# Performance work log

Measured on AMD Instinct MI355X. Metric: run time of the kernel, lower is better.

The kernel has to match this reference:

```python
import jax, jax.numpy as jnp
import numpy as np

HIDDEN = 32  # hidden_size


def setup_inputs() -> dict:
    key = jax.random.key(0)
    kx, kwx, kwh = jax.random.split(key, 3)
    B, T, F = 256, 2048, 64
    x = jax.random.normal(kx, (B, T, F), dtype=jnp.float32)
    # Flax OptimizedLSTMCell params: input kernel (no bias) and hidden kernel (with bias),
    # gate order (i, f, g, o), each of width HIDDEN -> concatenated 4*HIDDEN.
    Wx = jax.random.normal(kwx, (F, 4 * HIDDEN), dtype=jnp.float32) / np.sqrt(F)
    Wh = jax.random.normal(kwh, (HIDDEN, 4 * HIDDEN), dtype=jnp.float32) / np.sqrt(HIDDEN)
    b = jnp.zeros((4 * HIDDEN,), dtype=jnp.float32)
    return {"x": x, "Wx": Wx, "Wh": Wh, "b": b}


def _lstm(x, Wx, Wh, b):
    B, T, F = x.shape
    H = Wh.shape[0]
    # Precompute input contribution for all timesteps (same math, one big GEMM).
    xg = jnp.einsum("btf,fg->btg", x, Wx) + b  # [B, T, 4H]
    xg = xg.swapaxes(0, 1)  # [T, B, 4H] for scan over time
    c0 = jnp.zeros((B, H), dtype=x.dtype)
    h0 = jnp.zeros((B, H), dtype=x.dtype)

    def step(carry, xg_t):
        c, h = carry
        gates = xg_t + h @ Wh  # [B, 4H]
        i, f, g, o = jnp.split(gates, 4, axis=-1)  # flax gate order: i, f, g, o
        c_new = jax.nn.sigmoid(f) * c + jax.nn.sigmoid(i) * jnp.tanh(g)
        h_new = jax.nn.sigmoid(o) * jnp.tanh(c_new)
        return (c_new, h_new), h_new

    _, ys = jax.lax.scan(step, (c0, h0), xg)  # ys: [T, B, H]
    return ys.swapaxes(0, 1)  # [B, T, H]


def reference(x, Wx, Wh, b):
    return _lstm(x, Wx, Wh, b)
```

## Files before the change

kernel.cpp:

```cpp
#include <hip/hip_runtime.h>
#include <hip/hip_fp16.h>

#define BB 256
#define TT 2048
#define FF 64
#define HH 32
#define G4 128
#define K2E 1.4426950408889634f

typedef float f32x2 __attribute__((ext_vector_type(2)));

__device__ __forceinline__ float fast_rcp(float x){ return __builtin_amdgcn_rcpf(x); }
__device__ __forceinline__ float fast_exp2(float x){
#if __has_builtin(__builtin_amdgcn_exp2f)
  return __builtin_amdgcn_exp2f(x);
#else
  return exp2f(x);
#endif
}
__device__ __forceinline__ void swap_halves(float &a, float &b){
#if __has_builtin(__builtin_amdgcn_permlane32_swap)
  typedef int i32x2_ __attribute__((ext_vector_type(2)));
  i32x2_ r = __builtin_amdgcn_permlane32_swap(__float_as_int(a), __float_as_int(b), false, false);
  a = __int_as_float(r.x);
  b = __int_as_float(r.y);
#else
  asm("v_permlane32_swap_b32 %0, %1" : "+v"(a), "+v"(b));
#endif
}

#define PKFMA_VV(acc, a, b) asm("v_pk_fma_f32 %0, %1, %2, %0" : "+v"(acc) : "v"(a), "v"(b))
#define DOT2_SV(acc, hs, wv) asm("v_dot2_f32_f16 %0, %1, %2, %0" : "+v"(acc) : "s"(hs), "v"(wv))

__global__ __launch_bounds__(256) void lstm_gemm(const float* __restrict__ x,
    const float* __restrict__ Wx, const float* __restrict__ bias,
    float* __restrict__ xg, int t0, int ct)
{
  __shared__ float sW[FF*G4];
  __shared__ float sB[G4];
  __shared__ float sX[64*68];
  int tid = threadIdx.x;
  {
    const float4* Wx4 = (const float4*)Wx;
    float4* sW4 = (float4*)sW;
#pragma unroll
    for (int q=0;q<8;q++) sW4[q*256+tid] = Wx4[q*256+tid];
    if (tid < 32) ((float4*)sB)[tid] = ((const float4*)bias)[tid];
  }
  long total = (long)BB*ct;
  long m0 = (long)blockIdx.x * 64;
#pragma unroll
  for (int s=0;s<4;s++){
    int idx = tid + s*256;
    int row = idx >> 4, q = idx & 15;
    long gm = m0 + row;
    float4 v = make_float4(0.f,0.f,0.f,0.f);
    if (gm < total){
      int bidx = (int)((unsigned long)gm / (unsigned)ct);
      int tt   = (int)(gm - (long)bidx*ct);
      v = ((const float4*)(x + ((size_t)bidx*TT + t0 + tt)*FF))[q];
    }
    *(float4*)&sX[row*68 + q*4] = v;
  }
  __syncthreads();
  int rg = tid >> 5;
  int cg = tid & 31;
  int r0 = rg*8;
  f32x2 acc[8][4];
#pragma unroll
  for (int r=0;r<8;r++)
#pragma unroll
    for (int c=0;c<4;c++) acc[r][c] = (f32x2){0.f,0.f};
#pragma unroll 8
  for (int kp=0; kp<32; kp++){
    int k = kp*2;
    f32x2 xv[8];
#pragma unroll
    for (int r=0;r<8;r++) xv[r] = *(const f32x2*)&sX[(r0+r)*68 + k];
    f32x2 wv[4];
#pragma unroll
    for (int c=0;c<4;c++){
      f32x2 w; w.x = sW[k*G4 + cg + 32*c]; w.y = sW[(k+1)*G4 + cg + 32*c];
      wv[c] = w;
    }
#pragma unroll
    for (int r=0;r<8;r++)
#pragma unroll
      for (int c=0;c<4;c++) PKFMA_VV(acc[r][c], xv[r], wv[c]);
  }
#pragma unroll
  for (int r=0;r<8;r++){
    long gm = m0 + r0 + r;
    if (gm < total){
      f32x2* o = (f32x2*)(xg + (size_t)gm*G4);
      f32x2 p0, p1;
      p0.x = (acc[r][0].x + acc[r][0].y + sB[cg])      * (-K2E);
      p0.y = (acc[r][1].x + acc[r][1].y + sB[cg+32])   * (-K2E);
      p1.x = (acc[r][2].x + acc[r][2].y + sB[cg+64])   * (2.f*K2E);
      p1.y = (acc[r][3].x + acc[r][3].y + sB[cg+96])   * (-K2E);
      o[cg]      = p0;
      o[cg + 32] = p1;
    }
  }
}

__global__ __launch_bounds__(64)
__attribute__((amdgpu_waves_per_eu(1,1)))
void lstm_scan(const float* __restrict__ xg,
    const float* __restrict__ Wh, float* __restrict__ ys,
    float* __restrict__ state, int t0, int ct)
{
  int r = blockIdx.x;
  int l = threadIdx.x;
  int j = l & 31;
  int half = l >> 5;
  int base = j + half*64;

  float ws0 = half ? (2.f*K2E) : (-K2E);
  float ws1 = -K2E;
  unsigned wh0[16], wh1[16];
#pragma unroll
  for (int kk=0;kk<16;kk++){
    __half2 a  = __floats2half2_rn(Wh[(2*kk)*G4 + base]*ws0,    Wh[(2*kk+1)*G4 + base]*ws0);
    __half2 b_ = __floats2half2_rn(Wh[(2*kk)*G4 + base+32]*ws1, Wh[(2*kk+1)*G4 + base+32]*ws1);
    wh0[kk] = *(unsigned*)&a;
    wh1[kk] = *(unsigned*)&b_;
  }
#pragma unroll
  for (int kk=0;kk<16;kk++){ asm volatile("" : "+v"(wh0[kk]), "+v"(wh1[kk])); }

  float A0 = half ? -2.f : 1.f;
  float B0 = half ?  1.f : 0.f;

  float da = (float)half, db = (float)half;
  swap_halves(da, db);
  bool flip = (da != 0.0f);

  float cc, hcur;
  if (t0 == 0){ cc = 0.f; hcur = 0.f; }
  else { cc = state[r*HH + j]; hcur = state[BB*HH + r*HH + j]; }

  const f32x2* xq = (const f32x2*)(xg + (size_t)r*ct*G4) + l;
  float* yp = ys + ((size_t)r*TT + t0)*HH;

  auto STEP = [&](f32x2 xv, int t){
    float hn = __int_as_float(__builtin_amdgcn_update_dpp(
        0, __float_as_int(hcur), 0xB1 , 0xF, 0xF, true));
    __half2 pk2 = __floats2half2_rn(hcur, hn);
    int pk = *(int*)&pk2;
    int hp[16];
#pragma unroll
    for (int kk=0;kk<16;kk++) hp[kk] = __builtin_amdgcn_readlane(pk, 2*kk);
    float cA = xv.x, cB = 0.f, dA = xv.y, dB = 0.f;
#pragma unroll
    for (int kk=0;kk<8;kk++){
      DOT2_SV(cA, hp[kk],   wh0[kk]);
      DOT2_SV(dA, hp[kk],   wh1[kk]);
      DOT2_SV(cB, hp[kk+8], wh0[kk+8]);
      DOT2_SV(dB, hp[kk+8], wh1[kk+8]);
    }
    float g0 = cA + cB;
    float g1 = dA + dB;
    float t1v = fast_rcp(1.f + fast_exp2(g1));
    float t0v = fmaf(A0, fast_rcp(1.f + fast_exp2(g0)), B0);
    float si = t0v, tg = t0v;
    swap_halves(si, tg);
    float ig = si * tg;
    float e0 = t1v, e1 = t1v;
    swap_halves(e0, e1);
    float sf = flip ? e1 : e0;
    float so = flip ? e0 : e1;
    cc = fmaf(sf, cc, ig);
    float tc = fmaf(-2.f, fast_rcp(1.f + fast_exp2((2.f*K2E)*cc)), 1.f);
    hcur = so * tc;
    if (half == 0) yp[(size_t)t*HH + j] = hcur;
  };

  f32x2 bufA[8], bufB[8];
#pragma unroll
  for (int u=0;u<8;u++){ int t_ = (u < ct) ? u : (ct-1); bufA[u] = xq[(size_t)t_*64]; }

  int tb = 0;
  for (; tb + 16 <= ct; tb += 16){
#pragma unroll
    for (int u=0;u<8;u++) bufB[u] = xq[(size_t)(tb+8+u)*64];
#pragma unroll
    for (int u=0;u<8;u++) STEP(bufA[u], tb+u);
#pragma unroll
    for (int u=0;u<8;u++){ int t_ = tb+16+u; if (t_ > ct-1) t_ = ct-1; bufA[u] = xq[(size_t)t_*64]; }
#pragma unroll
    for (int u=0;u<8;u++) STEP(bufB[u], tb+8+u);
  }
  for (int t=tb; t<ct; ++t) STEP(xq[(size_t)t*64], t);

  if (half == 0){
    state[r*HH + j] = cc;
    state[BB*HH + r*HH + j] = hcur;
  }
}

extern "C" void kernel_launch(void* const* d_in, const int* in_sizes, int n_in,
                              void* d_out, int out_size, void* d_ws, size_t ws_size,
                              hipStream_t stream)
{
  const float* x  = (const float*)d_in[0];
  const float* Wx = (const float*)d_in[1];
  const float* Wh = (const float*)d_in[2];
  const float* b  = (const float*)d_in[3];
  float* ys = (float*)d_out;
  char* ws = (char*)d_ws;
  float* state = (float*)ws;
  float* xg = (float*)(ws + 65536);
  size_t per_step = (size_t)BB * G4 * sizeof(float);
  size_t avail = ws_size > 65536 ? ws_size - 65536 : 0;
  long ctl = (long)(avail / per_step);
  int CT = (ctl >= TT) ? TT : (int)ctl;
  if (CT < 1) CT = 1;
  for (int t0 = 0; t0 < TT; t0 += CT){
    int ct = (TT - t0 < CT) ? (TT - t0) : CT;
    int wgs = (int)(((long)BB*ct + 63)/64);
    lstm_gemm<<<dim3(wgs), dim3(256), 0, stream>>>(x, Wx, b, xg, t0, ct);
    lstm_scan<<<dim3(BB), dim3(64), 0, stream>>>(xg, Wh, ys, state, t0, ct);
  }
}
```

Baseline: 526.0 us.

## Process two batch rows per scan wavefront to interleave independent recurrences

```diff
diff --git a/kernel.cpp b/kernel.cpp
--- a/kernel.cpp
+++ b/kernel.cpp
@@ -110,7 +110,8 @@
     const float* __restrict__ Wh, float* __restrict__ ys,
     float* __restrict__ state, int t0, int ct)
 {
-  int r = blockIdx.x;
+  int rA = blockIdx.x * 2;
+  int rB = rA + 1;
   int l = threadIdx.x;
   int j = l & 31;
   int half = l >> 5;
@@ -136,67 +137,99 @@
   swap_halves(da, db);
   bool flip = (da != 0.0f);
 
-  float cc, hcur;
-  if (t0 == 0){ cc = 0.f; hcur = 0.f; }
-  else { cc = state[r*HH + j]; hcur = state[BB*HH + r*HH + j]; }
-
-  const f32x2* xq = (const f32x2*)(xg + (size_t)r*ct*G4) + l;
-  float* yp = ys + ((size_t)r*TT + t0)*HH;
-
-  auto STEP = [&](f32x2 xv, int t){
+  float ccA, hA, ccB, hB;
+  if (t0 == 0){ ccA = hA = ccB = hB = 0.f; }
+  else {
+    ccA = state[rA*HH + j];  hA = state[BB*HH + rA*HH + j];
+    ccB = state[rB*HH + j];  hB = state[BB*HH + rB*HH + j];
+  }
+
+  const f32x2* xqA = (const f32x2*)(xg + (size_t)rA*ct*G4) + l;
+  const f32x2* xqB = (const f32x2*)(xg + (size_t)rB*ct*G4) + l;
+  float* ypS = ys + ((size_t)(rA+half)*TT + t0)*HH + j;
+
+  auto PACK = [&](float h)->int{
     float hn = __int_as_float(__builtin_amdgcn_update_dpp(
-        0, __float_as_int(hcur), 0xB1 , 0xF, 0xF, true));
-    __half2 pk2 = __floats2half2_rn(hcur, hn);
-    int pk = *(int*)&pk2;
-    int hp[16];
-#pragma unroll
-    for (int kk=0;kk<16;kk++) hp[kk] = __builtin_amdgcn_readlane(pk, 2*kk);
-    float cA = xv.x, cB = 0.f, dA = xv.y, dB = 0.f;
+        0, __float_as_int(h), 0xB1 , 0xF, 0xF, true));
+    __half2 pk2 = __floats2half2_rn(h, hn);
+    return *(int*)&pk2;
+  };
+
+  auto STEP2 = [&](f32x2 xa, f32x2 xb, int t){
+    int pkA = PACK(hA);
+    int pkB = PACK(hB);
+    int hpA[16], hpB[16];
+#pragma unroll
+    for (int kk=0;kk<16;kk++){
+      hpA[kk] = __builtin_amdgcn_readlane(pkA, 2*kk);
+      hpB[kk] = __builtin_amdgcn_readlane(pkB, 2*kk);
+    }
+    float cA0=xa.x, cA1=0.f, dA0=xa.y, dA1=0.f;
+    float cB0=xb.x, cB1=0.f, dB0=xb.y, dB1=0.f;
 #pragma unroll
     for (int kk=0;kk<8;kk++){
-      DOT2_SV(cA, hp[kk],   wh0[kk]);
-      DOT2_SV(dA, hp[kk],   wh1[kk]);
-      DOT2_SV(cB, hp[kk+8], wh0[kk+8]);
-      DOT2_SV(dB, hp[kk+8], wh1[kk+8]);
-    }
-    float g0 = cA + cB;
-    float g1 = dA + dB;
-    float t1v = fast_rcp(1.f + fast_exp2(g1));
-    float t0v = fmaf(A0, fast_rcp(1.f + fast_exp2(g0)), B0);
-    float si = t0v, tg = t0v;
-    swap_halves(si, tg);
-    float ig = si * tg;
-    float e0 = t1v, e1 = t1v;
-    swap_halves(e0, e1);
-    float sf = flip ? e1 : e0;
-    float so = flip ? e0 : e1;
-    cc = fmaf(sf, cc, ig);
-    float tc = fmaf(-2.f, fast_rcp(1.f + fast_exp2((2.f*K2E)*cc)), 1.f);
-    hcur = so * tc;
-    if (half == 0) yp[(size_t)t*HH + j] = hcur;
+      DOT2_SV(cA0, hpA[kk],   wh0[kk]);
+      DOT2_SV(dA0, hpA[kk],   wh1[kk]);
+      DOT2_SV(cB0, hpB[kk],   wh0[kk]);
+      DOT2_SV(dB0, hpB[kk],   wh1[kk]);
+      DOT2_SV(cA1, hpA[kk+8], wh0[kk+8]);
+      DOT2_SV(dA1, hpA[kk+8], wh1[kk+8]);
+      DOT2_SV(cB1, hpB[kk+8], wh0[kk+8]);
+      DOT2_SV(dB1, hpB[kk+8], wh1[kk+8]);
+    }
+    float g0A = cA0+cA1, g1A = dA0+dA1;
+    float g0B = cB0+cB1, g1B = dB0+dB1;
+    float t1A = fast_rcp(1.f + fast_exp2(g1A));
+    float t1B = fast_rcp(1.f + fast_exp2(g1B));
+    float t0A = fmaf(A0, fast_rcp(1.f + fast_exp2(g0A)), B0);
+    float t0B = fmaf(A0, fast_rcp(1.f + fast_exp2(g0B)), B0);
+    float siA = t0A, tgA = t0A; swap_halves(siA, tgA);
+    float siB = t0B, tgB = t0B; swap_halves(siB, tgB);
+    float igA = siA * tgA;
+    float igB = siB * tgB;
+    float e0A = t1A, e1A = t1A; swap_halves(e0A, e1A);
+    float e0B = t1B, e1B = t1B; swap_halves(e0B, e1B);
+    float sfA = flip ? e1A : e0A, soA = flip ? e0A : e1A;
+    float sfB = flip ? e1B : e0B, soB = flip ? e0B : e1B;
+    ccA = fmaf(sfA, ccA, igA);
+    ccB = fmaf(sfB, ccB, igB);
+    float tcA = fmaf(-2.f, fast_rcp(1.f + fast_exp2((2.f*K2E)*ccA)), 1.f);
+    float tcB = fmaf(-2.f, fast_rcp(1.f + fast_exp2((2.f*K2E)*ccB)), 1.f);
+    hA = soA * tcA;
+    hB = soB * tcB;
+    ypS[(size_t)t*HH] = half ? hB : hA;
   };
 
-  f32x2 bufA[8], bufB[8];
-#pragma unroll
-  for (int u=0;u<8;u++){ int t_ = (u < ct) ? u : (ct-1); bufA[u] = xq[(size_t)t_*64]; }
-
+  f32x2 aA[4], aB[4], bA[4], bB[4];
+#pragma unroll
+  for (int u=0;u<4;u++){
+    int t_ = (u < ct) ? u : (ct-1);
+    aA[u] = xqA[(size_t)t_*64];
+    aB[u] = xqB[(size_t)t_*64];
+  }
   int tb = 0;
-  for (; tb + 16 <= ct; tb += 16){
-#pragma unroll
-    for (int u=0;u<8;u++) bufB[u] = xq[(size_t)(tb+8+u)*64];
-#pragma unroll
-    for (int u=0;u<8;u++) STEP(bufA[u], tb+u);
-#pragma unroll
-    for (int u=0;u<8;u++){ int t_ = tb+16+u; if (t_ > ct-1) t_ = ct-1; bufA[u] = xq[(size_t)t_*64]; }
-#pragma unroll
-    for (int u=0;u<8;u++) STEP(bufB[u], tb+8+u);
-  }
-  for (int t=tb; t<ct; ++t) STEP(xq[(size_t)t*64], t);
-
-  if (half == 0){
-    state[r*HH + j] = cc;
-    state[BB*HH + r*HH + j] = hcur;
-  }
+  for (; tb + 8 <= ct; tb += 8){
+#pragma unroll
+    for (int u=0;u<4;u++){
+      int t_ = tb + 4 + u;
+      bA[u] = xqA[(size_t)t_*64];
+      bB[u] = xqB[(size_t)t_*64];
+    }
+#pragma unroll
+    for (int u=0;u<4;u++) STEP2(aA[u], aB[u], tb+u);
+#pragma unroll
+    for (int u=0;u<4;u++){
+      int t_ = tb + 8 + u; if (t_ > ct-1) t_ = ct-1;
+      aA[u] = xqA[(size_t)t_*64];
+      aB[u] = xqB[(size_t)t_*64];
+    }
+#pragma unroll
+    for (int u=0;u<4;u++) STEP2(bA[u], bB[u], tb+4+u);
+  }
+  for (int t=tb; t<ct; ++t) STEP2(xqA[(size_t)t*64], xqB[(size_t)t*64], t);
+
+  state[(rA+half)*HH + j]         = half ? ccB : ccA;
+  state[BB*HH + (rA+half)*HH + j] = half ? hB  : hA;
 }
 
 extern "C" void kernel_launch(void* const* d_in, const int* in_sizes, int n_in,
@@ -220,6 +253,6 @@
     int ct = (TT - t0 < CT) ? (TT - t0) : CT;
     int wgs = (int)(((long)BB*ct + 63)/64);
     lstm_gemm<<<dim3(wgs), dim3(256), 0, stream>>>(x, Wx, b, xg, t0, ct);
-    lstm_scan<<<dim3(BB), dim3(64), 0, stream>>>(xg, Wh, ys, state, t0, ct);
-  }
-}
+    lstm_scan<<<dim3(BB/2), dim3(64), 0, stream>>>(xg, Wh, ys, state, t0, ct);
+  }
+}
```

Measured after the change: 786.7 us. 49.6% more time.
